# Kernel optimization log

Measured on AMD Instinct MI355X. Metric: run time of the kernel, lower is better.

Reference implementation:

```python
import jax, jax.numpy as jnp
import numpy as np

N_NODES = 100000
N_EDGES = 1600000
IN_FEATS = 128
N_HIDDEN = 128
N_CLASSES = 64


def _degree_norms(src, dst, n_nodes):
    ones = jnp.ones(src.shape[0], dtype=jnp.float32)
    deg_out = jax.ops.segment_sum(ones, src, num_segments=n_nodes)  # out-degree of src nodes
    deg_in = jax.ops.segment_sum(ones, dst, num_segments=n_nodes)   # in-degree of dst nodes
    norm_src = jax.lax.rsqrt(jnp.clip(deg_out, 1.0))  # D_src^{-1/2}, clamp like DGL
    norm_dst = jax.lax.rsqrt(jnp.clip(deg_in, 1.0))   # D_dst^{-1/2}
    return norm_src, norm_dst


def _graph_conv(x, src, dst, norm_src, norm_dst, W, b, relu):
    # DGL GraphConv, norm='both': D_dst^{-1/2} A D_src^{-1/2} X W + b
    h = x * norm_src[:, None]
    agg = jax.ops.segment_sum(h[src], dst, num_segments=x.shape[0])  # [N, d]
    h = agg * norm_dst[:, None]
    h = h @ W + b
    return jax.nn.relu(h) if relu else h


def setup_inputs() -> dict:
    key = jax.random.key(0)
    ks = jax.random.split(key, 10)
    features = jax.random.normal(ks[0], (N_NODES, IN_FEATS), dtype=jnp.float32)
    src = jax.random.randint(ks[1], (N_EDGES,), 0, N_NODES, dtype=jnp.int64 if jax.config.read('jax_enable_x64') else jnp.int32)
    dst = jax.random.randint(ks[2], (N_EDGES,), 0, N_NODES, dtype=src.dtype)
    s = 1.0 / np.sqrt(IN_FEATS)
    W0 = jax.random.uniform(ks[3], (IN_FEATS, N_HIDDEN), jnp.float32, -s, s)
    b0 = jnp.zeros((N_HIDDEN,), jnp.float32)
    sh = 1.0 / np.sqrt(N_HIDDEN)
    W1 = jax.random.uniform(ks[4], (N_HIDDEN, N_HIDDEN), jnp.float32, -sh, sh)
    b1 = jnp.zeros((N_HIDDEN,), jnp.float32)
    W2 = jax.random.uniform(ks[5], (N_HIDDEN, N_CLASSES), jnp.float32, -sh, sh)
    b2 = jnp.zeros((N_CLASSES,), jnp.float32)
    return {"features": features, "src": src, "dst": dst,
            "W0": W0, "b0": b0, "W1": W1, "b1": b1, "W2": W2, "b2": b2}


def reference(features, src, dst, W0, b0, W1, b1, W2, b2):
    norm_src, norm_dst = _degree_norms(src, dst, features.shape[0])
    # dropout is identity in eval mode
    h = _graph_conv(features, src, dst, norm_src, norm_dst, W0, b0, relu=True)
    h = _graph_conv(h, src, dst, norm_src, norm_dst, W1, b1, relu=True)
    h = _graph_conv(h, src, dst, norm_src, norm_dst, W2, b2, relu=False)
    return h
```

## Files before the change

### kernel.cpp

```cpp
#include <hip/hip_runtime.h>
#include <hip/hip_fp16.h>

#define K_FEATS 128
#define RBSHIFT 9
#define RB 512

typedef short bf16x8 __attribute__((ext_vector_type(8)));
typedef float f32x4 __attribute__((ext_vector_type(4)));

__device__ __forceinline__ unsigned short bf16_rne(float x) {
    unsigned u = __float_as_uint(x);
    unsigned r = (u + 0x7FFFu + ((u >> 16) & 1u)) >> 16;
    return (unsigned short)r;
}
__device__ __forceinline__ float bf16_f(unsigned short h) {
    return __uint_as_float(((unsigned)h) << 16);
}

__global__ __launch_bounds__(256) void count_split(
    const int* __restrict__ src, const int* __restrict__ dst,
    int* __restrict__ partialS, int* __restrict__ partialD,
    const float* __restrict__ W0, const float* __restrict__ W1,
    const float* __restrict__ W2,
    unsigned short* __restrict__ W0th, unsigned short* __restrict__ W0tl,
    unsigned short* __restrict__ W1th, unsigned short* __restrict__ W1tl,
    unsigned short* __restrict__ W2th, unsigned short* __restrict__ W2tl,
    int ne, int chunkA, int C, int NB)
{
    __shared__ int hS[256];
    __shared__ int hD[256];
    int bid = blockIdx.x, t = threadIdx.x;
    if (bid < C) {
        if (t < NB) { hS[t] = 0; hD[t] = 0; }
        __syncthreads();
        int e0 = bid * chunkA, e1 = min(ne, e0 + chunkA);
        for (int e = e0 + t; e < e1; e += 256) {
            atomicAdd(&hS[src[e] >> RBSHIFT], 1);
            atomicAdd(&hD[dst[e] >> RBSHIFT], 1);
        }
        __syncthreads();
        for (int i = t; i < NB; i += 256) {
            partialS[i * C + bid] = hS[i];
            partialD[i * C + bid] = hD[i];
        }
    } else {
        int e = (bid - C) * 256 + t;
        const float* W; unsigned short *Wh, *Wl; int NC, idx;
        bool ok = true;
        if (e < 16384)      { W = W0; Wh = W0th; Wl = W0tl; NC = 128; idx = e; }
        else if (e < 32768) { W = W1; Wh = W1th; Wl = W1tl; NC = 128; idx = e - 16384; }
        else if (e < 40960) { W = W2; Wh = W2th; Wl = W2tl; NC = 64;  idx = e - 32768; }
        else ok = false;
        if (ok) {
            int c = idx >> 7, kk = idx & 127;
            float w = W[kk * NC + c];
            unsigned short h = bf16_rne(w);
            Wh[idx] = h;
            Wl[idx] = bf16_rne(w - bf16_f(h));
        }
    }
}

__global__ __launch_bounds__(256) void bucket_prefix(
    int* __restrict__ partialS, int* __restrict__ partialD,
    int* __restrict__ totS, int* __restrict__ totD, int C, int NB)
{
    __shared__ int sh[256];
    int b = blockIdx.x, t = threadIdx.x;
    int* part = blockIdx.y ? partialD : partialS;
    int* tot = blockIdx.y ? totD : totS;
    int v = (t < C) ? part[b * C + t] : 0;
    sh[t] = v;
    __syncthreads();
    for (int off = 1; off < 256; off <<= 1) {
        int x = (t >= off) ? sh[t - off] : 0;
        __syncthreads();
        sh[t] += x;
        __syncthreads();
    }
    if (t < C) part[b * C + t] = sh[t] - v;
    if (t == 255) tot[b] = sh[255];
}

__global__ __launch_bounds__(256) void bucket_scatter(
    const int* __restrict__ src, const int* __restrict__ dst,
    const int* __restrict__ partialS, const int* __restrict__ partialD,
    const int* __restrict__ totS, const int* __restrict__ totD,
    unsigned short* __restrict__ src_bkt, int* __restrict__ edge_bkt,
    int ne, int chunkA, int C, int NB)
{
    __shared__ int shB[256];
    __shared__ int curS[256];
    __shared__ int curD[256];
    int bid = blockIdx.x, t = threadIdx.x;
    int vS = (t < NB) ? totS[t] : 0;
    shB[t] = vS;
    __syncthreads();
    for (int off = 1; off < 256; off <<= 1) {
        int x = (t >= off) ? shB[t - off] : 0;
        __syncthreads();
        shB[t] += x;
        __syncthreads();
    }
    if (t < NB) curS[t] = (shB[t] - vS) + partialS[t * C + bid];
    __syncthreads();
    int vD = (t < NB) ? totD[t] : 0;
    shB[t] = vD;
    __syncthreads();
    for (int off = 1; off < 256; off <<= 1) {
        int x = (t >= off) ? shB[t - off] : 0;
        __syncthreads();
        shB[t] += x;
        __syncthreads();
    }
    if (t < NB) curD[t] = (shB[t] - vD) + partialD[t * C + bid];
    __syncthreads();
    int e0 = bid * chunkA, e1 = min(ne, e0 + chunkA);
    for (int e = e0 + t; e < e1; e += 256) {
        int s = src[e];
        int d = dst[e];
        int posD = atomicAdd(&curD[d >> RBSHIFT], 1);
        edge_bkt[posD] = ((d & (RB - 1)) << 17) | s;
        int posS = atomicAdd(&curS[s >> RBSHIFT], 1);
        src_bkt[posS] = (unsigned short)(s & (RB - 1));
    }
}

__global__ __launch_bounds__(256) void fine_all(
    const int* __restrict__ edge_bkt, const unsigned short* __restrict__ src_bkt,
    const int* __restrict__ totS, const int* __restrict__ totD,
    int* __restrict__ row_off, float* __restrict__ norm_dst,
    float* __restrict__ norm_src, int* __restrict__ csr, int n, int ne, int NB)
{
    __shared__ int shA[RB];
    __shared__ int shB[256];
    int bid = blockIdx.x, t = threadIdx.x;
    int y = bid & 1, b = bid >> 1;
    const int* tot = y ? totS : totD;
    int v = (t < NB) ? tot[t] : 0;
    shB[t] = v;
    __syncthreads();
    for (int off = 1; off < 256; off <<= 1) {
        int x = (t >= off) ? shB[t - off] : 0;
        __syncthreads();
        shB[t] += x;
        __syncthreads();
    }
    int e1 = shB[b];
    int ebase = e1 - tot[b];
    __syncthreads();
    int lo = b << RBSHIFT;
    for (int i = t; i < RB; i += 256) shA[i] = 0;
    __syncthreads();
    if (y == 1) {
        for (int e = ebase + t; e < e1; e += 256)
            atomicAdd(&shA[src_bkt[e]], 1);
        __syncthreads();
        for (int i = t; i < RB; i += 256) {
            int g = lo + i;
            if (g < n) norm_src[g] = rsqrtf((float)max(shA[i], 1));
        }
        return;
    }
    if (bid == 0 && t == 0) row_off[n] = ne;
    for (int e = ebase + t; e < e1; e += 256)
        atomicAdd(&shA[(unsigned)edge_bkt[e] >> 17], 1);
    __syncthreads();
    int v0 = shA[2 * t], v1 = shA[2 * t + 1];
    shB[t] = v0 + v1;
    __syncthreads();
    for (int off = 1; off < 256; off <<= 1) {
        int x = (t >= off) ? shB[t - off] : 0;
        __syncthreads();
        shB[t] += x;
        __syncthreads();
    }
    int excl = shB[t] - (v0 + v1) + ebase;
    int g0 = lo + 2 * t, g1 = g0 + 1;
    if (g0 < n) { row_off[g0] = excl;      norm_dst[g0] = rsqrtf((float)max(v0, 1)); }
    if (g1 < n) { row_off[g1] = excl + v0; norm_dst[g1] = rsqrtf((float)max(v1, 1)); }
    shA[2 * t] = excl;
    shA[2 * t + 1] = excl + v0;
    __syncthreads();
    for (int e = ebase + t; e < e1; e += 256) {
        int p = edge_bkt[e];
        int pos = atomicAdd(&shA[(unsigned)p >> 17], 1);
        csr[pos] = p & 0x1FFFF;
    }
}

template <int NCOL, bool HALF_OUT, int MODE>
__global__ __launch_bounds__(256) void gemm_mfma(
    const __half* __restrict__ X16, const float* __restrict__ Xf,
    const unsigned short* __restrict__ Wth, const unsigned short* __restrict__ Wtl,
    const float* __restrict__ scale, void* __restrict__ outv, int n)
{
    constexpr int CT = NCOL / 16;
    constexpr int CHUNKS = NCOL * 16;
    __shared__ unsigned short Ws[16 * NCOL * 8];

    int t = threadIdx.x;
    int w = t >> 6, lane = t & 63, m = lane & 15, q = lane >> 4;
    int r0 = blockIdx.x * 128 + w * 32;

    f32x4 acc[2][CT];
#pragma unroll
    for (int i = 0; i < 2; i++)
#pragma unroll
        for (int j = 0; j < CT; j++) acc[i][j] = (f32x4){0.f, 0.f, 0.f, 0.f};

    bf16x8 ah[2][4], al[2][4];
#pragma unroll
    for (int rt = 0; rt < 2; rt++) {
        int row = r0 + rt * 16 + m;
        size_t base = (size_t)row * K_FEATS + q * 8;
#pragma unroll
        for (int k = 0; k < 4; k++) {
            float f[8];
            if (MODE == 0) {
                if (row < n) {
                    *(float4*)&f[0] = *(const float4*)(Xf + base + k * 32);
                    *(float4*)&f[4] = *(const float4*)(Xf + base + k * 32 + 4);
                } else {
#pragma unroll
                    for (int j = 0; j < 8; j++) f[j] = 0.f;
                }
            } else {
                union { uint4 q4; __half h[8]; } U;
                U.q4 = *(const uint4*)(X16 + base + k * 32);
#pragma unroll
                for (int j = 0; j < 8; j++) f[j] = __half2float(U.h[j]);
            }
            union { bf16x8 v; unsigned short u[8]; } H, L;
#pragma unroll
            for (int j = 0; j < 8; j++) {
                unsigned uf = __float_as_uint(f[j]);
                H.u[j] = (unsigned short)(uf >> 16);
                float r = f[j] - __uint_as_float(uf & 0xFFFF0000u);
                if (MODE == 1)
                    L.u[j] = (unsigned short)(__float_as_uint(r) >> 16);
                else
                    L.u[j] = bf16_rne(r);
            }
            ah[rt][k] = H.v;
            al[rt][k] = L.v;
        }
    }

#pragma unroll
    for (int i = 0; i < CHUNKS / 256; i++) {
        int g = t + i * 256;
        int col = g >> 4, sec = g & 15;
        *(bf16x8*)(Ws + sec * NCOL * 8 + ((col ^ (sec & 7)) * 8)) =
            *(const bf16x8*)(Wth + g * 8);
    }
    __syncthreads();
#pragma unroll
    for (int k = 0; k < 4; k++) {
        int sec = k * 4 + q;
#pragma unroll
        for (int ct = 0; ct < CT; ct++) {
            bf16x8 bh = *(const bf16x8*)(Ws + sec * NCOL * 8 +
                                         (((ct * 16 + m) ^ (sec & 7)) * 8));
            acc[0][ct] = __builtin_amdgcn_mfma_f32_16x16x32_bf16(ah[0][k], bh, acc[0][ct], 0, 0, 0);
            acc[0][ct] = __builtin_amdgcn_mfma_f32_16x16x32_bf16(al[0][k], bh, acc[0][ct], 0, 0, 0);
            acc[1][ct] = __builtin_amdgcn_mfma_f32_16x16x32_bf16(ah[1][k], bh, acc[1][ct], 0, 0, 0);
            acc[1][ct] = __builtin_amdgcn_mfma_f32_16x16x32_bf16(al[1][k], bh, acc[1][ct], 0, 0, 0);
        }
    }
    __syncthreads();
#pragma unroll
    for (int i = 0; i < CHUNKS / 256; i++) {
        int g = t + i * 256;
        int col = g >> 4, sec = g & 15;
        *(bf16x8*)(Ws + sec * NCOL * 8 + ((col ^ (sec & 7)) * 8)) =
            *(const bf16x8*)(Wtl + g * 8);
    }
    __syncthreads();
#pragma unroll
    for (int k = 0; k < 4; k++) {
        int sec = k * 4 + q;
#pragma unroll
        for (int ct = 0; ct < CT; ct++) {
            bf16x8 bl = *(const bf16x8*)(Ws + sec * NCOL * 8 +
                                         (((ct * 16 + m) ^ (sec & 7)) * 8));
            acc[0][ct] = __builtin_amdgcn_mfma_f32_16x16x32_bf16(ah[0][k], bl, acc[0][ct], 0, 0, 0);
            acc[1][ct] = __builtin_amdgcn_mfma_f32_16x16x32_bf16(ah[1][k], bl, acc[1][ct], 0, 0, 0);
        }
    }

#pragma unroll
    for (int rt = 0; rt < 2; rt++) {
        int rb = r0 + rt * 16 + q * 4;
#pragma unroll
        for (int reg = 0; reg < 4; reg++) {
            int row = rb + reg;
            if (row < n) {
                float s = scale[row];
#pragma unroll
                for (int ct = 0; ct < CT; ct++) {
                    float v = acc[rt][ct][reg] * s;
                    size_t o = (size_t)row * NCOL + ct * 16 + m;
                    if (HALF_OUT) ((__half*)outv)[o] = __float2half(v);
                    else ((float*)outv)[o] = v;
                }
            }
        }
    }
}

template <bool RELU>
__global__ __launch_bounds__(256) void aggregate4h(
    const __half* __restrict__ Tm, const int* __restrict__ row_off,
    const int* __restrict__ csr, const float* __restrict__ ndst,
    const float* __restrict__ bias, __half* __restrict__ Oh, int n)
{
    int lane = threadIdx.x & 15;
    int team = threadIdx.x >> 4;
    int fb = lane * 8;
    float b[8];
    *(float4*)&b[0] = *(const float4*)(bias + fb);
    *(float4*)&b[4] = *(const float4*)(bias + fb + 4);
    int stride = gridDim.x * 16;
    for (int v = blockIdx.x * 16 + team; v < n; v += stride) {
        int s = row_off[v], e = row_off[v + 1];
        float nd = ndst[v];
        float a[8] = {};
        int i = s;
        for (; i + 4 <= e; i += 4) {
            int u0 = csr[i], u1 = csr[i + 1], u2 = csr[i + 2], u3 = csr[i + 3];
            union { uint4 q; __half h[8]; } U0, U1, U2, U3;
            U0.q = *(const uint4*)(Tm + (size_t)u0 * 128 + fb);
            U1.q = *(const uint4*)(Tm + (size_t)u1 * 128 + fb);
            U2.q = *(const uint4*)(Tm + (size_t)u2 * 128 + fb);
            U3.q = *(const uint4*)(Tm + (size_t)u3 * 128 + fb);
#pragma unroll
            for (int j = 0; j < 8; j++)
                a[j] += (__half2float(U0.h[j]) + __half2float(U1.h[j])) +
                        (__half2float(U2.h[j]) + __half2float(U3.h[j]));
        }
        for (; i < e; i++) {
            int u = csr[i];
            union { uint4 q; __half h[8]; } U;
            U.q = *(const uint4*)(Tm + (size_t)u * 128 + fb);
#pragma unroll
            for (int j = 0; j < 8; j++) a[j] += __half2float(U.h[j]);
        }
        union { uint4 q; __half h[8]; } O;
#pragma unroll
        for (int j = 0; j < 8; j++) {
            float o = nd * a[j] + b[j];
            if (RELU) o = fmaxf(o, 0.f);
            O.h[j] = __float2half(o);
        }
        *(uint4*)(Oh + (size_t)v * 128 + fb) = O.q;
    }
}

__global__ __launch_bounds__(256) void aggregate2h(
    const __half* __restrict__ Tm, const int* __restrict__ row_off,
    const int* __restrict__ csr, const float* __restrict__ ndst,
    const float* __restrict__ bias, float* __restrict__ out, int n)
{
    int lane = threadIdx.x & 7;
    int team = threadIdx.x >> 3;
    int fb = lane * 8;
    float b[8];
    *(float4*)&b[0] = *(const float4*)(bias + fb);
    *(float4*)&b[4] = *(const float4*)(bias + fb + 4);
    int stride = gridDim.x * 32;
    for (int v = blockIdx.x * 32 + team; v < n; v += stride) {
        int s = row_off[v], e = row_off[v + 1];
        float nd = ndst[v];
        float a[8] = {};
        int i = s;
        for (; i + 4 <= e; i += 4) {
            int u0 = csr[i], u1 = csr[i + 1], u2 = csr[i + 2], u3 = csr[i + 3];
            union { uint4 q; __half h[8]; } U0, U1, U2, U3;
            U0.q = *(const uint4*)(Tm + (size_t)u0 * 64 + fb);
            U1.q = *(const uint4*)(Tm + (size_t)u1 * 64 + fb);
            U2.q = *(const uint4*)(Tm + (size_t)u2 * 64 + fb);
            U3.q = *(const uint4*)(Tm + (size_t)u3 * 64 + fb);
#pragma unroll
            for (int j = 0; j < 8; j++)
                a[j] += (__half2float(U0.h[j]) + __half2float(U1.h[j])) +
                        (__half2float(U2.h[j]) + __half2float(U3.h[j]));
        }
        for (; i < e; i++) {
            int u = csr[i];
            union { uint4 q; __half h[8]; } U;
            U.q = *(const uint4*)(Tm + (size_t)u * 64 + fb);
#pragma unroll
            for (int j = 0; j < 8; j++) a[j] += __half2float(U.h[j]);
        }
        float o[8];
#pragma unroll
        for (int j = 0; j < 8; j++) o[j] = nd * a[j] + b[j];
        *(float4*)(out + (size_t)v * 64 + fb) = *(float4*)&o[0];
        *(float4*)(out + (size_t)v * 64 + fb + 4) = *(float4*)&o[4];
    }
}

extern "C" void kernel_launch(void* const* d_in, const int* in_sizes, int n_in,
                              void* d_out, int out_size, void* d_ws, size_t ws_size,
                              hipStream_t stream)
{
    const float* features = (const float*)d_in[0];
    const int* src = (const int*)d_in[1];
    const int* dst = (const int*)d_in[2];
    const float* W0 = (const float*)d_in[3];
    const float* b0 = (const float*)d_in[4];
    const float* W1 = (const float*)d_in[5];
    const float* b1 = (const float*)d_in[6];
    const float* W2 = (const float*)d_in[7];
    const float* b2 = (const float*)d_in[8];

    int n = in_sizes[0] / K_FEATS;
    int ne = in_sizes[1];
    int n_pad = (n + 127) & ~127;

    char* ws = (char*)d_ws;
    size_t off = 0;
    auto take = [&](size_t bytes) -> char* {
        char* p = ws + off;
        off = (off + bytes + 255) & ~(size_t)255;
        return p;
    };
    __half* Xbuf = (__half*)take((size_t)n_pad * 128 * 2);
    __half* Th = (__half*)take((size_t)n_pad * 128 * 2);
    int* csr = (int*)take((size_t)ne * 4);
    int* edge_bkt = (int*)take((size_t)ne * 4);
    unsigned short* src_bkt = (unsigned short*)take((size_t)ne * 2);
    int* row_off = (int*)take((size_t)(n + 1) * 4);
    float* norm_src = (float*)take((size_t)n * 4);
    float* norm_dst = (float*)take((size_t)n * 4);
    unsigned short* W0th = (unsigned short*)take(128 * 128 * 2);
    unsigned short* W0tl = (unsigned short*)take(128 * 128 * 2);
    unsigned short* W1th = (unsigned short*)take(128 * 128 * 2);
    unsigned short* W1tl = (unsigned short*)take(128 * 128 * 2);
    unsigned short* W2th = (unsigned short*)take(64 * 128 * 2);
    unsigned short* W2tl = (unsigned short*)take(64 * 128 * 2);

    int NB = (n + RB - 1) >> RBSHIFT;
    int chunkA = 8192;
    int C = (ne + chunkA - 1) / chunkA;
    if (C > 256) { chunkA = (ne + 255) / 256; C = (ne + chunkA - 1) / chunkA; }

    int* partialS = (int*)take((size_t)NB * C * 4);
    int* partialD = (int*)take((size_t)NB * C * 4);
    int* totS = (int*)take((size_t)NB * 4);
    int* totD = (int*)take((size_t)NB * 4);

    count_split<<<C + 160, 256, 0, stream>>>(
        src, dst, partialS, partialD,
        W0, W1, W2, W0th, W0tl, W1th, W1tl, W2th, W2tl,
        ne, chunkA, C, NB);
    bucket_prefix<<<dim3(NB, 2), 256, 0, stream>>>(partialS, partialD, totS, totD, C, NB);
    bucket_scatter<<<C, 256, 0, stream>>>(src, dst, partialS, partialD,
                                          totS, totD, src_bkt, edge_bkt,
                                          ne, chunkA, C, NB);
    fine_all<<<2 * NB, 256, 0, stream>>>(edge_bkt, src_bkt, totS, totD,
                                         row_off, norm_dst, norm_src, csr,
                                         n, ne, NB);

    int gblocks = n_pad / 128;
    int ablocks4 = (n + 15) / 16;
    int ablocks2 = (n + 31) / 32;

    gemm_mfma<128, true, 0><<<gblocks, 256, 0, stream>>>(
        nullptr, features, W0th, W0tl, norm_src, Th, n);
    aggregate4h<true><<<ablocks4, 256, 0, stream>>>(Th, row_off, csr, norm_dst, b0,
                                                    Xbuf, n);
    gemm_mfma<128, true, 1><<<gblocks, 256, 0, stream>>>(
        Xbuf, nullptr, W1th, W1tl, norm_src, Th, n);
    aggregate4h<true><<<ablocks4, 256, 0, stream>>>(Th, row_off, csr, norm_dst, b1,
                                                    Xbuf, n);
    gemm_mfma<64, true, 1><<<gblocks, 256, 0, stream>>>(
        Xbuf, nullptr, W2th, W2tl, norm_src, Th, n);
    aggregate2h<<<ablocks2, 256, 0, stream>>>(Th, row_off, csr, norm_dst, b2,
                                              (float*)d_out, n);
}
```

Measured before the change: 374.9 us.

## Store intermediate features in 16-column slabs and aggregate per slab

Intermediate node features move from row-major [N,128] to slab-major layout: eight slabs of 16 halves per node, each slab contiguous over nodes. The GEMM writes and reads this layout, and the aggregation kernels now assign each block to one slab, gathering 8-byte pieces per neighbour from a 3.2MB slab. The goal is to keep each slab's gather working set in cache (L2/LLC) instead of scattering over the whole feature matrix, at the cost of smaller, less coalesced gather transactions and eight passes over the CSR indices. Aggregation launches a fixed grid of 2048 blocks in grid-stride loops.

After: 450.1 us. 1.2x slower.

```diff
diff --git a/kernel.cpp b/kernel.cpp
--- a/kernel.cpp
+++ b/kernel.cpp
@@ -193,7 +193,7 @@
 __global__ __launch_bounds__(256) void gemm_mfma(
     const __half* __restrict__ X16, const float* __restrict__ Xf,
     const unsigned short* __restrict__ Wth, const unsigned short* __restrict__ Wtl,
-    const float* __restrict__ scale, void* __restrict__ outv, int n)
+    const float* __restrict__ scale, void* __restrict__ outv, int n, int SS)
 {
     constexpr int CT = NCOL / 16;
     constexpr int CHUNKS = NCOL * 16;
@@ -213,11 +213,11 @@
 #pragma unroll
     for (int rt = 0; rt < 2; rt++) {
         int row = r0 + rt * 16 + m;
-        size_t base = (size_t)row * K_FEATS + q * 8;
 #pragma unroll
         for (int k = 0; k < 4; k++) {
             float f[8];
             if (MODE == 0) {
+                size_t base = (size_t)row * K_FEATS + q * 8;
                 if (row < n) {
                     *(float4*)&f[0] = *(const float4*)(Xf + base + k * 32);
                     *(float4*)&f[4] = *(const float4*)(Xf + base + k * 32 + 4);
@@ -226,8 +226,10 @@
                     for (int j = 0; j < 8; j++) f[j] = 0.f;
                 }
             } else {
+                size_t abase = (size_t)(2 * k + (q >> 1)) * SS +
+                               (size_t)row * 16 + (q & 1) * 8;
                 union { uint4 q4; __half h[8]; } U;
-                U.q4 = *(const uint4*)(X16 + base + k * 32);
+                U.q4 = *(const uint4*)(X16 + abase);
 #pragma unroll
                 for (int j = 0; j < 8; j++) f[j] = __half2float(U.h[j]);
             }
@@ -300,7 +302,7 @@
 #pragma unroll
                 for (int ct = 0; ct < CT; ct++) {
                     float v = acc[rt][ct][reg] * s;
-                    size_t o = (size_t)row * NCOL + ct * 16 + m;
+                    size_t o = (size_t)ct * SS + (size_t)row * 16 + m;
                     if (HALF_OUT) ((__half*)outv)[o] = __float2half(v);
                     else ((float*)outv)[o] = v;
                 }
@@ -310,94 +312,95 @@
 }
 
 template <bool RELU>
-__global__ __launch_bounds__(256) void aggregate4h(
+__global__ __launch_bounds__(256) void aggregate4s(
     const __half* __restrict__ Tm, const int* __restrict__ row_off,
     const int* __restrict__ csr, const float* __restrict__ ndst,
-    const float* __restrict__ bias, __half* __restrict__ Oh, int n)
-{
-    int lane = threadIdx.x & 15;
-    int team = threadIdx.x >> 4;
-    int fb = lane * 8;
-    float b[8];
-    *(float4*)&b[0] = *(const float4*)(bias + fb);
-    *(float4*)&b[4] = *(const float4*)(bias + fb + 4);
-    int stride = gridDim.x * 16;
-    for (int v = blockIdx.x * 16 + team; v < n; v += stride) {
-        int s = row_off[v], e = row_off[v + 1];
+    const float* __restrict__ bias, __half* __restrict__ Oh, int n, int SS)
+{
+    int lane = threadIdx.x & 3;
+    int team = threadIdx.x >> 2;
+    int s = blockIdx.x & 7;
+    int ch = blockIdx.x >> 3;
+    int nch = gridDim.x >> 3;
+    const __half* Ts = Tm + (size_t)s * SS + lane * 4;
+    __half* Os = Oh + (size_t)s * SS + lane * 4;
+    float b[4];
+    *(float4*)b = *(const float4*)(bias + s * 16 + lane * 4);
+    int stride = nch * 64;
+    for (int v = ch * 64 + team; v < n; v += stride) {
+        int i = row_off[v], e = row_off[v + 1];
         float nd = ndst[v];
-        float a[8] = {};
-        int i = s;
+        float a[4] = {};
         for (; i + 4 <= e; i += 4) {
             int u0 = csr[i], u1 = csr[i + 1], u2 = csr[i + 2], u3 = csr[i + 3];
-            union { uint4 q; __half h[8]; } U0, U1, U2, U3;
-            U0.q = *(const uint4*)(Tm + (size_t)u0 * 128 + fb);
-            U1.q = *(const uint4*)(Tm + (size_t)u1 * 128 + fb);
-            U2.q = *(const uint4*)(Tm + (size_t)u2 * 128 + fb);
-            U3.q = *(const uint4*)(Tm + (size_t)u3 * 128 + fb);
-#pragma unroll
-            for (int j = 0; j < 8; j++)
-                a[j] += (__half2float(U0.h[j]) + __half2float(U1.h[j])) +
-                        (__half2float(U2.h[j]) + __half2float(U3.h[j]));
+            union { uint2 q; __half h[4]; } A, B, C, D;
+            A.q = *(const uint2*)(Ts + (size_t)u0 * 16);
+            B.q = *(const uint2*)(Ts + (size_t)u1 * 16);
+            C.q = *(const uint2*)(Ts + (size_t)u2 * 16);
+            D.q = *(const uint2*)(Ts + (size_t)u3 * 16);
+#pragma unroll
+            for (int j = 0; j < 4; j++)
+                a[j] += (__half2float(A.h[j]) + __half2float(B.h[j])) +
+                        (__half2float(C.h[j]) + __half2float(D.h[j]));
         }
         for (; i < e; i++) {
-            int u = csr[i];
-            union { uint4 q; __half h[8]; } U;
-            U.q = *(const uint4*)(Tm + (size_t)u * 128 + fb);
-#pragma unroll
-            for (int j = 0; j < 8; j++) a[j] += __half2float(U.h[j]);
-        }
-        union { uint4 q; __half h[8]; } O;
-#pragma unroll
-        for (int j = 0; j < 8; j++) {
+            union { uint2 q; __half h[4]; } A;
+            A.q = *(const uint2*)(Ts + (size_t)csr[i] * 16);
+#pragma unroll
+            for (int j = 0; j < 4; j++) a[j] += __half2float(A.h[j]);
+        }
+        union { uint2 q; __half h[4]; } O;
+#pragma unroll
+        for (int j = 0; j < 4; j++) {
             float o = nd * a[j] + b[j];
             if (RELU) o = fmaxf(o, 0.f);
             O.h[j] = __float2half(o);
         }
-        *(uint4*)(Oh + (size_t)v * 128 + fb) = O.q;
-    }
-}
-
-__global__ __launch_bounds__(256) void aggregate2h(
+        *(uint2*)(Os + (size_t)v * 16) = O.q;
+    }
+}
+
+__global__ __launch_bounds__(256) void aggregate2s(
     const __half* __restrict__ Tm, const int* __restrict__ row_off,
     const int* __restrict__ csr, const float* __restrict__ ndst,
-    const float* __restrict__ bias, float* __restrict__ out, int n)
-{
-    int lane = threadIdx.x & 7;
-    int team = threadIdx.x >> 3;
-    int fb = lane * 8;
-    float b[8];
-    *(float4*)&b[0] = *(const float4*)(bias + fb);
-    *(float4*)&b[4] = *(const float4*)(bias + fb + 4);
-    int stride = gridDim.x * 32;
-    for (int v = blockIdx.x * 32 + team; v < n; v += stride) {
-        int s = row_off[v], e = row_off[v + 1];
+    const float* __restrict__ bias, float* __restrict__ out, int n, int SS)
+{
+    int lane = threadIdx.x & 3;
+    int team = threadIdx.x >> 2;
+    int r = blockIdx.x & 7;
+    int s = r >> 1;
+    int ch = (blockIdx.x >> 3) * 2 + (r & 1);
+    int nch = (gridDim.x >> 3) * 2;
+    const __half* Ts = Tm + (size_t)s * SS + lane * 4;
+    float b[4];
+    *(float4*)b = *(const float4*)(bias + s * 16 + lane * 4);
+    int stride = nch * 64;
+    for (int v = ch * 64 + team; v < n; v += stride) {
+        int i = row_off[v], e = row_off[v + 1];
         float nd = ndst[v];
-        float a[8] = {};
-        int i = s;
+        float a[4] = {};
         for (; i + 4 <= e; i += 4) {
             int u0 = csr[i], u1 = csr[i + 1], u2 = csr[i + 2], u3 = csr[i + 3];
-            union { uint4 q; __half h[8]; } U0, U1, U2, U3;
-            U0.q = *(const uint4*)(Tm + (size_t)u0 * 64 + fb);
-            U1.q = *(const uint4*)(Tm + (size_t)u1 * 64 + fb);
-            U2.q = *(const uint4*)(Tm + (size_t)u2 * 64 + fb);
-            U3.q = *(const uint4*)(Tm + (size_t)u3 * 64 + fb);
-#pragma unroll
-            for (int j = 0; j < 8; j++)
-                a[j] += (__half2float(U0.h[j]) + __half2float(U1.h[j])) +
-                        (__half2float(U2.h[j]) + __half2float(U3.h[j]));
+            union { uint2 q; __half h[4]; } A, B, C, D;
+            A.q = *(const uint2*)(Ts + (size_t)u0 * 16);
+            B.q = *(const uint2*)(Ts + (size_t)u1 * 16);
+            C.q = *(const uint2*)(Ts + (size_t)u2 * 16);
+            D.q = *(const uint2*)(Ts + (size_t)u3 * 16);
+#pragma unroll
+            for (int j = 0; j < 4; j++)
+                a[j] += (__half2float(A.h[j]) + __half2float(B.h[j])) +
+                        (__half2float(C.h[j]) + __half2float(D.h[j]));
         }
         for (; i < e; i++) {
-            int u = csr[i];
-            union { uint4 q; __half h[8]; } U;
-            U.q = *(const uint4*)(Tm + (size_t)u * 64 + fb);
-#pragma unroll
-            for (int j = 0; j < 8; j++) a[j] += __half2float(U.h[j]);
-        }
-        float o[8];
-#pragma unroll
-        for (int j = 0; j < 8; j++) o[j] = nd * a[j] + b[j];
-        *(float4*)(out + (size_t)v * 64 + fb) = *(float4*)&o[0];
-        *(float4*)(out + (size_t)v * 64 + fb + 4) = *(float4*)&o[4];
+            union { uint2 q; __half h[4]; } A;
+            A.q = *(const uint2*)(Ts + (size_t)csr[i] * 16);
+#pragma unroll
+            for (int j = 0; j < 4; j++) a[j] += __half2float(A.h[j]);
+        }
+        float o[4];
+#pragma unroll
+        for (int j = 0; j < 4; j++) o[j] = nd * a[j] + b[j];
+        *(float4*)(out + (size_t)v * 64 + s * 16 + lane * 4) = *(float4*)o;
     }
 }
 
@@ -418,6 +421,7 @@
     int n = in_sizes[0] / K_FEATS;
     int ne = in_sizes[1];
     int n_pad = (n + 127) & ~127;
+    int SS = n_pad * 16;
 
     char* ws = (char*)d_ws;
     size_t off = 0;
@@ -464,19 +468,18 @@
                                          n, ne, NB);
 
     int gblocks = n_pad / 128;
-    int ablocks4 = (n + 15) / 16;
-    int ablocks2 = (n + 31) / 32;
+    int agg_blocks = 2048;
 
     gemm_mfma<128, true, 0><<<gblocks, 256, 0, stream>>>(
-        nullptr, features, W0th, W0tl, norm_src, Th, n);
-    aggregate4h<true><<<ablocks4, 256, 0, stream>>>(Th, row_off, csr, norm_dst, b0,
-                                                    Xbuf, n);
+        nullptr, features, W0th, W0tl, norm_src, Th, n, SS);
+    aggregate4s<true><<<agg_blocks, 256, 0, stream>>>(Th, row_off, csr, norm_dst,
+                                                      b0, Xbuf, n, SS);
     gemm_mfma<128, true, 1><<<gblocks, 256, 0, stream>>>(
-        Xbuf, nullptr, W1th, W1tl, norm_src, Th, n);
-    aggregate4h<true><<<ablocks4, 256, 0, stream>>>(Th, row_off, csr, norm_dst, b1,
-                                                    Xbuf, n);
+        Xbuf, nullptr, W1th, W1tl, norm_src, Th, n, SS);
+    aggregate4s<true><<<agg_blocks, 256, 0, stream>>>(Th, row_off, csr, norm_dst,
+                                                      b1, Xbuf, n, SS);
     gemm_mfma<64, true, 1><<<gblocks, 256, 0, stream>>>(
-        Xbuf, nullptr, W2th, W2tl, norm_src, Th, n);
-    aggregate2h<<<ablocks2, 256, 0, stream>>>(Th, row_off, csr, norm_dst, b2,
-                                              (float*)d_out, n);
-}
+        Xbuf, nullptr, W2th, W2tl, norm_src, Th, n, SS);
+    aggregate2s<<<agg_blocks, 256, 0, stream>>>(Th, row_off, csr, norm_dst, b2,
+                                                (float*)d_out, n, SS);
+}
```

## Overlap layer-0 GEMM with CSR construction by splitting it across preprocessing kernels

Applied to the files above, without the earlier changes.

The first-layer feature GEMM is split into extra thread blocks appended to the bucket_prefix, bucket_scatter and fine_all launches, so it runs alongside graph preprocessing instead of as its own kernel. Because norm_src is not yet available during that GEMM, the source normalization moves into the first aggregation, which now loads nsrc per neighbor and scales each gathered row. This removes one launch and fills idle GPU capacity during the small preprocessing kernels. In exchange, the first aggregation does an extra gather and multiply per edge, and the GEMM blocks add LDS (shared memory) use that may lower occupancy of the co-scheduled kernels.

Result: no change. 371.9 us (-0.8%).

```diff
diff --git a/kernel.cpp b/kernel.cpp
--- a/kernel.cpp
+++ b/kernel.cpp
@@ -15,6 +15,108 @@
 }
 __device__ __forceinline__ float bf16_f(unsigned short h) {
     return __uint_as_float(((unsigned)h) << 16);
+}
+
+__device__ __forceinline__ void gemm0_block(
+    int gb, const float* __restrict__ Xf,
+    const unsigned short* __restrict__ Wth, const unsigned short* __restrict__ Wtl,
+    __half* __restrict__ outp, int n)
+{
+    __shared__ unsigned short Ws[16 * 128 * 8];
+    int t = threadIdx.x;
+    int w = t >> 6, lane = t & 63, m = lane & 15, q = lane >> 4;
+    int r0 = gb * 128 + w * 32;
+
+    f32x4 acc[2][8];
+#pragma unroll
+    for (int i = 0; i < 2; i++)
+#pragma unroll
+        for (int j = 0; j < 8; j++) acc[i][j] = (f32x4){0.f, 0.f, 0.f, 0.f};
+
+    bf16x8 ah[2][4], al[2][4];
+#pragma unroll
+    for (int rt = 0; rt < 2; rt++) {
+        int row = r0 + rt * 16 + m;
+        size_t base = (size_t)row * K_FEATS + q * 8;
+#pragma unroll
+        for (int k = 0; k < 4; k++) {
+            float f[8];
+            if (row < n) {
+                *(float4*)&f[0] = *(const float4*)(Xf + base + k * 32);
+                *(float4*)&f[4] = *(const float4*)(Xf + base + k * 32 + 4);
+            } else {
+#pragma unroll
+                for (int j = 0; j < 8; j++) f[j] = 0.f;
+            }
+            union { bf16x8 v; unsigned short u[8]; } H, L;
+#pragma unroll
+            for (int j = 0; j < 8; j++) {
+                unsigned uf = __float_as_uint(f[j]);
+                H.u[j] = (unsigned short)(uf >> 16);
+                float r = f[j] - __uint_as_float(uf & 0xFFFF0000u);
+                L.u[j] = bf16_rne(r);
+            }
+            ah[rt][k] = H.v;
+            al[rt][k] = L.v;
+        }
+    }
+
+#pragma unroll
+    for (int i = 0; i < 8; i++) {
+        int g = t + i * 256;
+        int col = g >> 4, sec = g & 15;
+        *(bf16x8*)(Ws + sec * 128 * 8 + ((col ^ (sec & 7)) * 8)) =
+            *(const bf16x8*)(Wth + g * 8);
+    }
+    __syncthreads();
+#pragma unroll
+    for (int k = 0; k < 4; k++) {
+        int sec = k * 4 + q;
+#pragma unroll
+        for (int ct = 0; ct < 8; ct++) {
+            bf16x8 bh = *(const bf16x8*)(Ws + sec * 128 * 8 +
+                                         (((ct * 16 + m) ^ (sec & 7)) * 8));
+            acc[0][ct] = __builtin_amdgcn_mfma_f32_16x16x32_bf16(ah[0][k], bh, acc[0][ct], 0, 0, 0);
+            acc[0][ct] = __builtin_amdgcn_mfma_f32_16x16x32_bf16(al[0][k], bh, acc[0][ct], 0, 0, 0);
+            acc[1][ct] = __builtin_amdgcn_mfma_f32_16x16x32_bf16(ah[1][k], bh, acc[1][ct], 0, 0, 0);
+            acc[1][ct] = __builtin_amdgcn_mfma_f32_16x16x32_bf16(al[1][k], bh, acc[1][ct], 0, 0, 0);
+        }
+    }
+    __syncthreads();
+#pragma unroll
+    for (int i = 0; i < 8; i++) {
+        int g = t + i * 256;
+        int col = g >> 4, sec = g & 15;
+        *(bf16x8*)(Ws + sec * 128 * 8 + ((col ^ (sec & 7)) * 8)) =
+            *(const bf16x8*)(Wtl + g * 8);
+    }
+    __syncthreads();
+#pragma unroll
+    for (int k = 0; k < 4; k++) {
+        int sec = k * 4 + q;
+#pragma unroll
+        for (int ct = 0; ct < 8; ct++) {
+            bf16x8 bl = *(const bf16x8*)(Ws + sec * 128 * 8 +
+                                         (((ct * 16 + m) ^ (sec & 7)) * 8));
+            acc[0][ct] = __builtin_amdgcn_mfma_f32_16x16x32_bf16(ah[0][k], bl, acc[0][ct], 0, 0, 0);
+            acc[1][ct] = __builtin_amdgcn_mfma_f32_16x16x32_bf16(ah[1][k], bl, acc[1][ct], 0, 0, 0);
+        }
+    }
+
+#pragma unroll
+    for (int rt = 0; rt < 2; rt++) {
+        int rb = r0 + rt * 16 + q * 4;
+#pragma unroll
+        for (int reg = 0; reg < 4; reg++) {
+            int row = rb + reg;
+            if (row < n) {
+#pragma unroll
+                for (int ct = 0; ct < 8; ct++)
+                    outp[(size_t)row * 128 + ct * 16 + m] =
+                        __float2half(acc[rt][ct][reg]);
+            }
+        }
+    }
 }
 
 __global__ __launch_bounds__(256) void count_split(
@@ -63,12 +165,19 @@
 
 __global__ __launch_bounds__(256) void bucket_prefix(
     int* __restrict__ partialS, int* __restrict__ partialD,
-    int* __restrict__ totS, int* __restrict__ totD, int C, int NB)
+    int* __restrict__ totS, int* __restrict__ totD, int C, int NB,
+    const float* __restrict__ Xf, const unsigned short* __restrict__ W0th,
+    const unsigned short* __restrict__ W0tl, __half* __restrict__ Th, int n)
 {
     __shared__ int sh[256];
-    int b = blockIdx.x, t = threadIdx.x;
-    int* part = blockIdx.y ? partialD : partialS;
-    int* tot = blockIdx.y ? totD : totS;
+    int bid = blockIdx.x, t = threadIdx.x;
+    if (bid >= 2 * NB) {
+        gemm0_block(bid - 2 * NB, Xf, W0th, W0tl, Th, n);
+        return;
+    }
+    int b = bid >> 1;
+    int* part = (bid & 1) ? partialD : partialS;
+    int* tot = (bid & 1) ? totD : totS;
     int v = (t < C) ? part[b * C + t] : 0;
     sh[t] = v;
     __syncthreads();
@@ -87,12 +196,19 @@
     const int* __restrict__ partialS, const int* __restrict__ partialD,
     const int* __restrict__ totS, const int* __restrict__ totD,
     unsigned short* __restrict__ src_bkt, int* __restrict__ edge_bkt,
-    int ne, int chunkA, int C, int NB)
+    int ne, int chunkA, int C, int NB,
+    const float* __restrict__ Xf, const unsigned short* __restrict__ W0th,
+    const unsigned short* __restrict__ W0tl, __half* __restrict__ Th,
+    int n, int G1)
 {
     __shared__ int shB[256];
     __shared__ int curS[256];
     __shared__ int curD[256];
     int bid = blockIdx.x, t = threadIdx.x;
+    if (bid >= C) {
+        gemm0_block(bid - C + G1, Xf, W0th, W0tl, Th, n);
+        return;
+    }
     int vS = (t < NB) ? totS[t] : 0;
     shB[t] = vS;
     __syncthreads();
@@ -130,11 +246,17 @@
     const int* __restrict__ edge_bkt, const unsigned short* __restrict__ src_bkt,
     const int* __restrict__ totS, const int* __restrict__ totD,
     int* __restrict__ row_off, float* __restrict__ norm_dst,
-    float* __restrict__ norm_src, int* __restrict__ csr, int n, int ne, int NB)
+    float* __restrict__ norm_src, int* __restrict__ csr, int n, int ne, int NB,
+    const float* __restrict__ Xf, const unsigned short* __restrict__ W0th,
+    const unsigned short* __restrict__ W0tl, __half* __restrict__ Th, int G12)
 {
     __shared__ int shA[RB];
     __shared__ int shB[256];
     int bid = blockIdx.x, t = threadIdx.x;
+    if (bid >= 2 * NB) {
+        gemm0_block(bid - 2 * NB + G12, Xf, W0th, W0tl, Th, n);
+        return;
+    }
     int y = bid & 1, b = bid >> 1;
     const int* tot = y ? totS : totD;
     int v = (t < NB) ? tot[t] : 0;
@@ -309,10 +431,11 @@
     }
 }
 
-template <bool RELU>
+template <bool RELU, bool NSRC>
 __global__ __launch_bounds__(256) void aggregate4h(
     const __half* __restrict__ Tm, const int* __restrict__ row_off,
     const int* __restrict__ csr, const float* __restrict__ ndst,
+    const float* __restrict__ nsrc,
     const float* __restrict__ bias, __half* __restrict__ Oh, int n)
 {
     int lane = threadIdx.x & 15;
@@ -334,17 +457,31 @@
             U1.q = *(const uint4*)(Tm + (size_t)u1 * 128 + fb);
             U2.q = *(const uint4*)(Tm + (size_t)u2 * 128 + fb);
             U3.q = *(const uint4*)(Tm + (size_t)u3 * 128 + fb);
-#pragma unroll
-            for (int j = 0; j < 8; j++)
-                a[j] += (__half2float(U0.h[j]) + __half2float(U1.h[j])) +
-                        (__half2float(U2.h[j]) + __half2float(U3.h[j]));
+            if (NSRC) {
+                float s0 = nsrc[u0], s1 = nsrc[u1], s2 = nsrc[u2], s3 = nsrc[u3];
+#pragma unroll
+                for (int j = 0; j < 8; j++)
+                    a[j] += (s0 * __half2float(U0.h[j]) + s1 * __half2float(U1.h[j])) +
+                            (s2 * __half2float(U2.h[j]) + s3 * __half2float(U3.h[j]));
+            } else {
+#pragma unroll
+                for (int j = 0; j < 8; j++)
+                    a[j] += (__half2float(U0.h[j]) + __half2float(U1.h[j])) +
+                            (__half2float(U2.h[j]) + __half2float(U3.h[j]));
+            }
         }
         for (; i < e; i++) {
             int u = csr[i];
             union { uint4 q; __half h[8]; } U;
             U.q = *(const uint4*)(Tm + (size_t)u * 128 + fb);
-#pragma unroll
-            for (int j = 0; j < 8; j++) a[j] += __half2float(U.h[j]);
+            if (NSRC) {
+                float s0 = nsrc[u];
+#pragma unroll
+                for (int j = 0; j < 8; j++) a[j] += s0 * __half2float(U.h[j]);
+            } else {
+#pragma unroll
+                for (int j = 0; j < 8; j++) a[j] += __half2float(U.h[j]);
+            }
         }
         union { uint4 q; __half h[8]; } O;
 #pragma unroll
@@ -451,30 +588,34 @@
     int* totS = (int*)take((size_t)NB * 4);
     int* totD = (int*)take((size_t)NB * 4);
 
+    int gblocks = n_pad / 128;
+    int G1 = 128;
+    int G2 = (gblocks - G1) / 2;
+    int G3 = gblocks - G1 - G2;
+
     count_split<<<C + 160, 256, 0, stream>>>(
         src, dst, partialS, partialD,
         W0, W1, W2, W0th, W0tl, W1th, W1tl, W2th, W2tl,
         ne, chunkA, C, NB);
-    bucket_prefix<<<dim3(NB, 2), 256, 0, stream>>>(partialS, partialD, totS, totD, C, NB);
-    bucket_scatter<<<C, 256, 0, stream>>>(src, dst, partialS, partialD,
-                                          totS, totD, src_bkt, edge_bkt,
-                                          ne, chunkA, C, NB);
-    fine_all<<<2 * NB, 256, 0, stream>>>(edge_bkt, src_bkt, totS, totD,
-                                         row_off, norm_dst, norm_src, csr,
-                                         n, ne, NB);
-
-    int gblocks = n_pad / 128;
+    bucket_prefix<<<2 * NB + G1, 256, 0, stream>>>(
+        partialS, partialD, totS, totD, C, NB,
+        features, W0th, W0tl, Th, n);
+    bucket_scatter<<<C + G2, 256, 0, stream>>>(
+        src, dst, partialS, partialD, totS, totD, src_bkt, edge_bkt,
+        ne, chunkA, C, NB, features, W0th, W0tl, Th, n, G1);
+    fine_all<<<2 * NB + G3, 256, 0, stream>>>(
+        edge_bkt, src_bkt, totS, totD, row_off, norm_dst, norm_src, csr,
+        n, ne, NB, features, W0th, W0tl, Th, G1 + G2);
+
     int ablocks4 = (n + 15) / 16;
     int ablocks2 = (n + 31) / 32;
 
-    gemm_mfma<128, true, 0><<<gblocks, 256, 0, stream>>>(
-        nullptr, features, W0th, W0tl, norm_src, Th, n);
-    aggregate4h<true><<<ablocks4, 256, 0, stream>>>(Th, row_off, csr, norm_dst, b0,
-                                                    Xbuf, n);
+    aggregate4h<true, true><<<ablocks4, 256, 0, stream>>>(
+        Th, row_off, csr, norm_dst, norm_src, b0, Xbuf, n);
     gemm_mfma<128, true, 1><<<gblocks, 256, 0, stream>>>(
         Xbuf, nullptr, W1th, W1tl, norm_src, Th, n);
-    aggregate4h<true><<<ablocks4, 256, 0, stream>>>(Th, row_off, csr, norm_dst, b1,
-                                                    Xbuf, n);
+    aggregate4h<true, false><<<ablocks4, 256, 0, stream>>>(
+        Th, row_off, csr, norm_dst, nullptr, b1, Xbuf, n);
     gemm_mfma<64, true, 1><<<gblocks, 256, 0, stream>>>(
         Xbuf, nullptr, W2th, W2tl, norm_src, Th, n);
     aggregate2h<<<ablocks2, 256, 0, stream>>>(Th, row_off, csr, norm_dst, b2,
```
